# Optimization experiments

Measured on AMD Instinct MI355X. Metric: run time of the kernel, lower is better.

The kernel has to match this reference:

```python
import jax, jax.numpy as jnp
import numpy as np

IN_F, OUT_F = 2048, 2048
IQ, OQ = IN_F // 4, OUT_F // 4
B, S = 4, 4096


def _xavier(key, shape):
    fan_out, fan_in = shape
    limit = float(np.sqrt(6.0 / (fan_in + fan_out)))
    return jax.random.uniform(key, shape, jnp.float32, -limit, limit)


def setup_inputs() -> dict:
    key = jax.random.key(0)
    kx, kr, ki, kj, kk = jax.random.split(key, 5)
    return {
        "x": jax.random.normal(kx, (B, S, IN_F), dtype=jnp.float32),
        "wr": _xavier(kr, (OQ, IQ)),
        "wi": _xavier(ki, (OQ, IQ)),
        "wj": _xavier(kj, (OQ, IQ)),
        "wk": _xavier(kk, (OQ, IQ)),
        "bias": jnp.zeros((OUT_F,), dtype=jnp.float32),
    }


def reference(x, wr, wi, wj, wk, bias):
    b, s, _ = x.shape
    iq = wr.shape[1]
    oq = wr.shape[0]
    # strided quaternion component extraction: x[..., c::4] -> (B*S, iq)
    xq = x.reshape(b * s, iq, 4)  # last-dim interleaved layout
    xr, xi, xj, xk = xq[..., 0], xq[..., 1], xq[..., 2], xq[..., 3]
    # small GEMMs against W^T (W is (oq, iq)); only the products actually used
    Ar = xr @ wr.T
    Br = xi @ wr.T
    Cr = xj @ wr.T
    Dr = xk @ wr.T
    Ai = xr @ wi.T
    Bi = xi @ wi.T
    Aj = xr @ wj.T
    Cj = xj @ wj.T
    Ak = xr @ wk.T
    Dk = xk @ wk.T
    # combine exactly as in the original module
    or_ = Ar - Bi - Cj - Dk
    oi_ = Br + Ai + Dk - Cj
    oj_ = Cr - Dk + Aj + Bi
    ok_ = Dr + Cj - Bi + Ak
    # interleaved scatter: out[:, c::4] = o<c>
    out = jnp.stack([or_, oi_, oj_, ok_], axis=-1).reshape(b, s, 4 * oq)
    return out + bias[None, None, :]
```

## Files before the change

### kernel.cpp

```cpp
#include <hip/hip_runtime.h>


typedef unsigned short u16;
typedef __bf16 bf16x8 __attribute__((ext_vector_type(8)));
typedef float f32x4 __attribute__((ext_vector_type(4)));

#define QM 16384
#define QN 2048
#define QK 2048

__device__ __forceinline__ u16 f2bf(float f) {
    union { float f; unsigned u; } v;
    v.f = f;
    unsigned r = v.u + 0x7FFFu + ((v.u >> 16) & 1u);
    return (u16)(r >> 16);
}

__device__ __forceinline__ void async_copy16(const u16* g, u16* l) {
    __builtin_amdgcn_global_load_lds(
        (const __attribute__((address_space(1))) void*)g,
        (__attribute__((address_space(3))) void*)l,
        16, 0, 0);
}

__global__ void cvt_x_kernel(const float* __restrict__ x, u16* __restrict__ y, int n4) {
    for (int i = blockIdx.x * blockDim.x + threadIdx.x; i < n4; i += gridDim.x * blockDim.x) {
        float4 v = reinterpret_cast<const float4*>(x)[i];
        ushort4 o;
        o.x = f2bf(v.x); o.y = f2bf(v.y); o.z = f2bf(v.z); o.w = f2bf(v.w);
        reinterpret_cast<ushort4*>(y)[i] = o;
    }
}

__global__ void pack_w_kernel(const float* __restrict__ wr, const float* __restrict__ wi,
                              const float* __restrict__ wj, const float* __restrict__ wk,
                              u16* __restrict__ W) {
    int i = blockIdx.x * blockDim.x + threadIdx.x;
    if (i >= QN * (QK / 4)) return;
    int n = i >> 9;
    int p = i & 511;
    int q = n >> 2, co = n & 3;
    int base = (q << 9) + p;
    float r  = wr[base], ii = wi[base], jj = wj[base], kk = wk[base];
    float e0, e1, e2, e3;
    if      (co == 0) { e0 = r;  e1 = -ii; e2 = -jj; e3 = -kk; }
    else if (co == 1) { e0 = ii; e1 = r;   e2 = -jj; e3 = kk;  }
    else if (co == 2) { e0 = jj; e1 = ii;  e2 = r;   e3 = -kk; }
    else              { e0 = kk; e1 = -ii; e2 = jj;  e3 = r;   }
    ushort4 o;
    o.x = f2bf(e0); o.y = f2bf(e1); o.z = f2bf(e2); o.w = f2bf(e3);
    reinterpret_cast<ushort4*>(W)[(n << 9) + p] = o;
}

__global__ __launch_bounds__(512, 2) void qgemm_kernel(const u16* __restrict__ A,
                                                       const u16* __restrict__ B,
                                                       const float* __restrict__ bias,
                                                       float* __restrict__ C) {
    __shared__ __align__(16) u16 L[81920];

    const int bid = blockIdx.x;
    const int swz = (bid & 7) * 64 + (bid >> 3);
    const int bm = swz >> 3;
    const int bn = swz & 7;

    const int tid = threadIdx.x;
    const int wid = tid >> 6, lane = tid & 63;
    const int wm = wid >> 2, wn = wid & 3;
    const int lr = lane & 15, lg = lane >> 4;

    const u16* Asrc = A + (size_t)bm * 256 * QK;
    const u16* Bsrc = B + (size_t)bn * 256 * QK;

    const int rA  = tid >> 3;
    const int clA = ((tid & 7) ^ (rA & 7)) << 3;
    const size_t soff = (size_t)rA * QK + clA;

    f32x4 acc[8][4];
#pragma unroll
    for (int i = 0; i < 8; ++i)
#pragma unroll
        for (int j = 0; j < 4; ++j)
            acc[i][j] = (f32x4){0.f, 0.f, 0.f, 0.f};

    auto stage = [&](const u16* src, int lbase, int k0) {
#pragma unroll
        for (int o = 0; o < 2; ++o)
            async_copy16(src + (size_t)(o * 64) * QK + k0 + soff,
                         &L[lbase + o * 4096 + wid * 512]);
    };

    auto rdA = [&](const u16* LA, int mf, int ks) -> bf16x8 {
        const int r = wm * 128 + mf * 16 + lr;
        const int c = ((ks * 4 + lg) ^ (r & 7)) << 3;
        return *(const bf16x8*)&LA[r * 64 + c];
    };
    auto rdB = [&](const u16* LB, int nf, int ks) -> bf16x8 {
        const int r = wn * 64 + nf * 16 + lr;
        const int c = ((ks * 4 + lg) ^ (r & 7)) << 3;
        return *(const bf16x8*)&LB[r * 64 + c];
    };

    auto doTile = [&](const int ab, const int bt, const int bt2, const int t)
        __attribute__((always_inline)) {
        const u16* LA = &L[ab * 16384];
        const u16* LB = &L[32768 + bt * 16384];
        const int tw1 = (t + 1) & 31, tw2 = (t + 2) & 31;
        const int oA = (ab ^ 1) * 16384;
        const int oB = 32768 + bt2 * 16384;

        bf16x8 a0[4], a1[4], b0[4], b1[4];

#pragma unroll
        for (int nf = 0; nf < 4; ++nf) b0[nf] = rdB(LB, nf, 0);
#pragma unroll
        for (int mf = 0; mf < 4; ++mf) a0[mf] = rdA(LA, mf, 0);
        stage(Asrc, oA, tw1 * 64);
        __builtin_amdgcn_s_setprio(1);
#pragma unroll
        for (int mf = 0; mf < 4; ++mf)
#pragma unroll
            for (int nf = 0; nf < 4; ++nf)
                acc[mf][nf] = __builtin_amdgcn_mfma_f32_16x16x32_bf16(a0[mf], b0[nf], acc[mf][nf], 0, 0, 0);
        __builtin_amdgcn_s_setprio(0);

#pragma unroll
        for (int mf = 0; mf < 4; ++mf) a1[mf] = rdA(LA, 4 + mf, 0);
#pragma unroll
        for (int nf = 0; nf < 4; ++nf) b1[nf] = rdB(LB, nf, 1);
        stage(Asrc + 128 * QK, oA + 8192, tw1 * 64);
        __builtin_amdgcn_s_setprio(1);
#pragma unroll
        for (int mf = 0; mf < 4; ++mf)
#pragma unroll
            for (int nf = 0; nf < 4; ++nf)
                acc[4 + mf][nf] = __builtin_amdgcn_mfma_f32_16x16x32_bf16(a1[mf], b0[nf], acc[4 + mf][nf], 0, 0, 0);
        __builtin_amdgcn_s_setprio(0);

#pragma unroll
        for (int mf = 0; mf < 4; ++mf) a0[mf] = rdA(LA, mf, 1);
        stage(Bsrc, oB, tw2 * 64);
        __builtin_amdgcn_s_setprio(1);
#pragma unroll
        for (int mf = 0; mf < 4; ++mf)
#pragma unroll
            for (int nf = 0; nf < 4; ++nf)
                acc[mf][nf] = __builtin_amdgcn_mfma_f32_16x16x32_bf16(a0[mf], b1[nf], acc[mf][nf], 0, 0, 0);
        __builtin_amdgcn_s_setprio(0);

#pragma unroll
        for (int mf = 0; mf < 4; ++mf) a1[mf] = rdA(LA, 4 + mf, 1);
        stage(Bsrc + 128 * QK, oB + 8192, tw2 * 64);
        __builtin_amdgcn_s_setprio(1);
#pragma unroll
        for (int mf = 0; mf < 4; ++mf)
#pragma unroll
            for (int nf = 0; nf < 4; ++nf)
                acc[4 + mf][nf] = __builtin_amdgcn_mfma_f32_16x16x32_bf16(a1[mf], b1[nf], acc[4 + mf][nf], 0, 0, 0);
        __builtin_amdgcn_s_setprio(0);

        asm volatile("s_waitcnt lgkmcnt(0) vmcnt(4)" ::: "memory");
        __builtin_amdgcn_s_barrier();
    };

    stage(Asrc,            0,             0);
    stage(Asrc + 128 * QK, 8192,          0);
    stage(Bsrc,            32768,             0);
    stage(Bsrc + 128 * QK, 32768 + 8192,      0);
    stage(Bsrc,            32768 + 16384,        64);
    stage(Bsrc + 128 * QK, 32768 + 16384 + 8192, 64);
    asm volatile("s_waitcnt vmcnt(4)" ::: "memory");
    __builtin_amdgcn_s_barrier();

    {
        int bt = 0, bt2 = 2;
        for (int t = 0; t < 32; ++t) {
            doTile(t & 1, bt, bt2, t);
            bt  = (bt  == 2) ? 0 : bt  + 1;
            bt2 = (bt2 == 2) ? 0 : bt2 + 1;
        }
    }

    const int colbase = bn * 256 + wn * 64;
    const int rowbase = bm * 256 + wm * 128;
    float bsv[4];
#pragma unroll
    for (int nf = 0; nf < 4; ++nf) bsv[nf] = bias[colbase + nf * 16 + lr];
    float* Cb = C + (size_t)rowbase * QN + colbase;
#pragma unroll
    for (int mf = 0; mf < 8; ++mf)
#pragma unroll
        for (int nf = 0; nf < 4; ++nf)
#pragma unroll
            for (int v = 0; v < 4; ++v)
                Cb[(size_t)(mf * 16 + lg * 4 + v) * QN + nf * 16 + lr] = acc[mf][nf][v] + bsv[nf];
}

extern "C" void kernel_launch(void* const* d_in, const int* in_sizes, int n_in,
                              void* d_out, int out_size, void* d_ws, size_t ws_size,
                              hipStream_t stream) {
    const float* x    = (const float*)d_in[0];
    const float* wr   = (const float*)d_in[1];
    const float* wi   = (const float*)d_in[2];
    const float* wj   = (const float*)d_in[3];
    const float* wk   = (const float*)d_in[4];
    const float* bias = (const float*)d_in[5];
    float* out = (float*)d_out;

    u16* xb = (u16*)d_ws;
    u16* wb = (u16*)((char*)d_ws + (size_t)QM * QK * 2);

    cvt_x_kernel<<<4096, 256, 0, stream>>>(x, xb, (QM * QK) / 4);
    pack_w_kernel<<<4096, 256, 0, stream>>>(wr, wi, wj, wk, wb);
    qgemm_kernel<<<512, 512, 0, stream>>>(xb, wb, bias, out);
}
```

Baseline: 163.1 us.

## Merge prep kernels, drop setprio, unroll tile loop by six

Folds the x conversion and weight packing into one prep kernel, with the block range deciding which job each block does. This removes one launch and lets the two jobs overlap. It also removes the s_setprio calls around the MFMA blocks. The main loop is manually unrolled by six so the buffer indices become compile-time constants, which removes the modulo bookkeeping and dynamic LDS address math, at the cost of larger code.

```diff
diff --git a/kernel.cpp b/kernel.cpp
--- a/kernel.cpp
+++ b/kernel.cpp
@@ -23,33 +23,35 @@
         16, 0, 0);
 }
 
-__global__ void cvt_x_kernel(const float* __restrict__ x, u16* __restrict__ y, int n4) {
-    for (int i = blockIdx.x * blockDim.x + threadIdx.x; i < n4; i += gridDim.x * blockDim.x) {
-        float4 v = reinterpret_cast<const float4*>(x)[i];
+__global__ void prep_kernel(const float* __restrict__ x, u16* __restrict__ xb,
+                            const float* __restrict__ wr, const float* __restrict__ wi,
+                            const float* __restrict__ wj, const float* __restrict__ wk,
+                            u16* __restrict__ wb) {
+    const int b = blockIdx.x;
+    if (b < 4096) {
+        const int n4 = (QM * QK) / 4;
+        for (int i = b * blockDim.x + threadIdx.x; i < n4; i += 4096 * blockDim.x) {
+            float4 v = reinterpret_cast<const float4*>(x)[i];
+            ushort4 o;
+            o.x = f2bf(v.x); o.y = f2bf(v.y); o.z = f2bf(v.z); o.w = f2bf(v.w);
+            reinterpret_cast<ushort4*>(xb)[i] = o;
+        }
+    } else {
+        int i = (b - 4096) * blockDim.x + threadIdx.x;
+        int n = i >> 9;
+        int p = i & 511;
+        int q = n >> 2, co = n & 3;
+        int base = (q << 9) + p;
+        float r  = wr[base], ii = wi[base], jj = wj[base], kk = wk[base];
+        float e0, e1, e2, e3;
+        if      (co == 0) { e0 = r;  e1 = -ii; e2 = -jj; e3 = -kk; }
+        else if (co == 1) { e0 = ii; e1 = r;   e2 = -jj; e3 = kk;  }
+        else if (co == 2) { e0 = jj; e1 = ii;  e2 = r;   e3 = -kk; }
+        else              { e0 = kk; e1 = -ii; e2 = jj;  e3 = r;   }
         ushort4 o;
-        o.x = f2bf(v.x); o.y = f2bf(v.y); o.z = f2bf(v.z); o.w = f2bf(v.w);
-        reinterpret_cast<ushort4*>(y)[i] = o;
+        o.x = f2bf(e0); o.y = f2bf(e1); o.z = f2bf(e2); o.w = f2bf(e3);
+        reinterpret_cast<ushort4*>(wb)[(n << 9) + p] = o;
     }
-}
-
-__global__ void pack_w_kernel(const float* __restrict__ wr, const float* __restrict__ wi,
-                              const float* __restrict__ wj, const float* __restrict__ wk,
-                              u16* __restrict__ W) {
-    int i = blockIdx.x * blockDim.x + threadIdx.x;
-    if (i >= QN * (QK / 4)) return;
-    int n = i >> 9;
-    int p = i & 511;
-    int q = n >> 2, co = n & 3;
-    int base = (q << 9) + p;
-    float r  = wr[base], ii = wi[base], jj = wj[base], kk = wk[base];
-    float e0, e1, e2, e3;
-    if      (co == 0) { e0 = r;  e1 = -ii; e2 = -jj; e3 = -kk; }
-    else if (co == 1) { e0 = ii; e1 = r;   e2 = -jj; e3 = kk;  }
-    else if (co == 2) { e0 = jj; e1 = ii;  e2 = r;   e3 = -kk; }
-    else              { e0 = kk; e1 = -ii; e2 = jj;  e3 = r;   }
-    ushort4 o;
-    o.x = f2bf(e0); o.y = f2bf(e1); o.z = f2bf(e2); o.w = f2bf(e3);
-    reinterpret_cast<ushort4*>(W)[(n << 9) + p] = o;
 }
 
 __global__ __launch_bounds__(512, 2) void qgemm_kernel(const u16* __restrict__ A,
@@ -115,48 +117,40 @@
 #pragma unroll
         for (int mf = 0; mf < 4; ++mf) a0[mf] = rdA(LA, mf, 0);
         stage(Asrc, oA, tw1 * 64);
-        __builtin_amdgcn_s_setprio(1);
 #pragma unroll
         for (int mf = 0; mf < 4; ++mf)
 #pragma unroll
             for (int nf = 0; nf < 4; ++nf)
                 acc[mf][nf] = __builtin_amdgcn_mfma_f32_16x16x32_bf16(a0[mf], b0[nf], acc[mf][nf], 0, 0, 0);
-        __builtin_amdgcn_s_setprio(0);
 
 #pragma unroll
         for (int mf = 0; mf < 4; ++mf) a1[mf] = rdA(LA, 4 + mf, 0);
 #pragma unroll
         for (int nf = 0; nf < 4; ++nf) b1[nf] = rdB(LB, nf, 1);
         stage(Asrc + 128 * QK, oA + 8192, tw1 * 64);
-        __builtin_amdgcn_s_setprio(1);
 #pragma unroll
         for (int mf = 0; mf < 4; ++mf)
 #pragma unroll
             for (int nf = 0; nf < 4; ++nf)
                 acc[4 + mf][nf] = __builtin_amdgcn_mfma_f32_16x16x32_bf16(a1[mf], b0[nf], acc[4 + mf][nf], 0, 0, 0);
-        __builtin_amdgcn_s_setprio(0);
 
 #pragma unroll
         for (int mf = 0; mf < 4; ++mf) a0[mf] = rdA(LA, mf, 1);
         stage(Bsrc, oB, tw2 * 64);
-        __builtin_amdgcn_s_setprio(1);
 #pragma unroll
         for (int mf = 0; mf < 4; ++mf)
 #pragma unroll
             for (int nf = 0; nf < 4; ++nf)
                 acc[mf][nf] = __builtin_amdgcn_mfma_f32_16x16x32_bf16(a0[mf], b1[nf], acc[mf][nf], 0, 0, 0);
-        __builtin_amdgcn_s_setprio(0);
 
 #pragma unroll
         for (int mf = 0; mf < 4; ++mf) a1[mf] = rdA(LA, 4 + mf, 1);
         stage(Bsrc + 128 * QK, oB + 8192, tw2 * 64);
-        __builtin_amdgcn_s_setprio(1);
 #pragma unroll
         for (int mf = 0; mf < 4; ++mf)
 #pragma unroll
             for (int nf = 0; nf < 4; ++nf)
                 acc[4 + mf][nf] = __builtin_amdgcn_mfma_f32_16x16x32_bf16(a1[mf], b1[nf], acc[4 + mf][nf], 0, 0, 0);
-        __builtin_amdgcn_s_setprio(0);
 
         asm volatile("s_waitcnt lgkmcnt(0) vmcnt(4)" ::: "memory");
         __builtin_amdgcn_s_barrier();
@@ -171,14 +165,16 @@
     asm volatile("s_waitcnt vmcnt(4)" ::: "memory");
     __builtin_amdgcn_s_barrier();
 
-    {
-        int bt = 0, bt2 = 2;
-        for (int t = 0; t < 32; ++t) {
-            doTile(t & 1, bt, bt2, t);
-            bt  = (bt  == 2) ? 0 : bt  + 1;
-            bt2 = (bt2 == 2) ? 0 : bt2 + 1;
-        }
+    for (int t = 0; t < 30; t += 6) {
+        doTile(0, 0, 2, t);
+        doTile(1, 1, 0, t + 1);
+        doTile(0, 2, 1, t + 2);
+        doTile(1, 0, 2, t + 3);
+        doTile(0, 1, 0, t + 4);
+        doTile(1, 2, 1, t + 5);
     }
+    doTile(0, 0, 2, 30);
+    doTile(1, 1, 0, 31);
 
     const int colbase = bn * 256 + wn * 64;
     const int rowbase = bm * 256 + wm * 128;
@@ -209,7 +205,6 @@
     u16* xb = (u16*)d_ws;
     u16* wb = (u16*)((char*)d_ws + (size_t)QM * QK * 2);
 
-    cvt_x_kernel<<<4096, 256, 0, stream>>>(x, xb, (QM * QK) / 4);
-    pack_w_kernel<<<4096, 256, 0, stream>>>(wr, wi, wj, wk, wb);
+    prep_kernel<<<8192, 256, 0, stream>>>(x, xb, wr, wi, wj, wk, wb);
     qgemm_kernel<<<512, 512, 0, stream>>>(xb, wb, bias, out);
 }
```

Result: faster. 159.1 us (-2.4%).
